# Kernel tuning notes

Measured on AMD Instinct MI355X. Metric: run time of the kernel, lower is better.

Reference implementation:

```python
import jax, jax.numpy as jnp
import numpy as np

B, T, D = 2, 4096, 1024      # batch, seq, hidden_dim
E, I = 16, 512               # n_routed_experts, expert_intermediate
K = 2                        # n_activated_experts
IS = 2048                    # shared_expert_intermediate
ALPHA = 1e-4                 # balance_loss_alpha
EPS = 1e-9


def setup_inputs() -> dict:
    key = jax.random.key(0)
    ks = jax.random.split(key, 8)
    s = lambda k, shape, fan: jax.random.normal(k, shape, jnp.float32) * (fan ** -0.5)
    return {
        "x": jax.random.normal(ks[0], (B, T, D), jnp.float32),
        "gate_w": s(ks[1], (D, E), D),            # router gate (no bias)
        "expert_bias": jnp.zeros((E,), jnp.float32),
        "sh_gate": s(ks[2], (D, IS), D),          # shared expert SwiGLU
        "sh_up": s(ks[3], (D, IS), D),
        "sh_down": s(ks[4], (IS, D), IS),
        "ex_gate": s(ks[5], (E, D, I), D),        # routed experts (stacked)
        "ex_up": s(ks[6], (E, D, I), D),
        "ex_down": s(ks[7], (E, I, D), I),
    }


def _swiglu(x, wg, wu, wd):
    return (jax.nn.silu(x @ wg) * (x @ wu)) @ wd


def reference(x, gate_w, expert_bias, sh_gate, sh_up, sh_down, ex_gate, ex_up, ex_down):
    Bq, Tq, Dq = x.shape
    # shared expert path (n_shared_experts = 1)
    shared = _swiglu(x, sh_gate, sh_up, sh_down)

    xf = x.reshape(Bq * Tq, Dq)                       # (N, D)
    N = xf.shape[0]

    # --- router: sigmoid gating, bias-adjusted top-k, normalized gates ---
    affinity = jax.nn.sigmoid(xf @ gate_w)            # (N, E)
    scores = affinity + expert_bias[None, :]
    _, idx = jax.lax.top_k(scores, K)                 # (N, K) int
    gv = jnp.take_along_axis(affinity, idx, axis=1)   # (N, K) gathered from affinity
    gv = gv / (gv.sum(-1, keepdims=True) + EPS)

    # --- balance loss (sequence-wise, Eq. 17-20) ---
    expert_mask = jax.nn.one_hot(idx, E, dtype=jnp.float32).sum(1)  # (N, E)
    f = expert_mask.sum(0) * E / (K * N)
    P = (affinity / (affinity.sum(-1, keepdims=True) + EPS)).mean(0)
    balance_loss = ALPHA * (f * P).sum()
    expert_counts = expert_mask.sum(0).astype(jnp.int32)            # (E,)

    # --- dispatch/compute/combine, expressed as dense combine-weight matrix ---
    # w[n, e] = sum of gate values for token n routed to expert e (same math
    # as the masked gather/scatter loop in the original)
    w = jnp.zeros((N, E), jnp.float32).at[jnp.arange(N)[:, None], idx].add(gv)
    h = jax.nn.silu(jnp.einsum('nd,edi->eni', xf, ex_gate)) \
        * jnp.einsum('nd,edi->eni', xf, ex_up)        # (E, N, I)
    routed = jnp.einsum('ne,eni,eid->nd', w, h, ex_down)  # (N, D)
    routed = routed.reshape(Bq, Tq, Dq)

    output = shared + routed  # note: original does NOT add residual despite docstring
    return output, balance_loss, expert_counts
```

## Files before the change

### kernel.cpp

```cpp
#include <hip/hip_runtime.h>
#include <stdint.h>

#define NTOK 8192
#define DDIM 1024
#define NEXP 16
#define KSEL 2
#define ISH 2048
#define IEX 512
#define ALPHAC 1e-4f
#define REPS 1e-9f

typedef __attribute__((ext_vector_type(8))) short short8;
typedef __attribute__((ext_vector_type(4))) float f32x4;

__device__ __forceinline__ unsigned short f2bf(float f){
  union { float f; uint32_t u; } v; v.f = f;
  uint32_t u = v.u;
  uint32_t r = (u + 0x7fffu + ((u >> 16) & 1u)) >> 16;
  return (unsigned short)r;
}
__device__ __forceinline__ float bf2f(unsigned short h){
  union { uint32_t u; float f; } v; v.u = ((uint32_t)h) << 16; return v.f;
}

__device__ __forceinline__ void gload16(const void* g, void* l){
  __builtin_amdgcn_global_load_lds(
      (const __attribute__((address_space(1))) void*)g,
      (__attribute__((address_space(3))) void*)l, 16, 0, 0);
}

__global__ __launch_bounds__(256) void convert_f32_bf16(const float* __restrict__ in,
                                                        unsigned short* __restrict__ out){
  int id = blockIdx.x * 256 + threadIdx.x;
  float4 v = ((const float4*)in)[id];
  ushort4 o;
  o.x = f2bf(v.x); o.y = f2bf(v.y); o.z = f2bf(v.z); o.w = f2bf(v.w);
  ((ushort4*)out)[id] = o;
}

__global__ __launch_bounds__(256) void transpose_bf16(const float* __restrict__ in,
                                                      unsigned short* __restrict__ outp,
                                                      int R, int C){
  __shared__ float tile[64][65];
  const size_t bofs = (size_t)blockIdx.z * R * C;
  const float* ip = in + bofs;
  unsigned short* op = outp + bofs;
  int c0 = blockIdx.x * 64, r0 = blockIdx.y * 64;
  int t = threadIdx.x;
  int tr = t >> 4, tc = (t & 15) * 4;
  #pragma unroll
  for (int i = 0; i < 4; ++i){
    float4 v = *(const float4*)&ip[(size_t)(r0 + tr + i*16) * C + c0 + tc];
    tile[tr + i*16][tc+0] = v.x;
    tile[tr + i*16][tc+1] = v.y;
    tile[tr + i*16][tc+2] = v.z;
    tile[tr + i*16][tc+3] = v.w;
  }
  __syncthreads();
  #pragma unroll
  for (int i = 0; i < 4; ++i){
    int oc = tr + i*16;
    ushort4 w;
    w.x = f2bf(tile[tc+0][oc]);
    w.y = f2bf(tile[tc+1][oc]);
    w.z = f2bf(tile[tc+2][oc]);
    w.w = f2bf(tile[tc+3][oc]);
    *(ushort4*)&op[(size_t)(c0 + oc) * R + r0 + tc] = w;
  }
}

__global__ __launch_bounds__(256) void logits_kernel(
    const float* __restrict__ x, const float* __restrict__ gw,
    float* __restrict__ logits)
{
  __shared__ float gws[16][1024];
  const int t = threadIdx.x;
  #pragma unroll
  for (int k = 0; k < 16; ++k){
    int idx = t + k * 256;
    float4 v = ((const float4*)gw)[idx];
    int d = idx >> 2, e0 = (idx & 3) * 4;
    gws[e0+0][d] = v.x;
    gws[e0+1][d] = v.y;
    gws[e0+2][d] = v.z;
    gws[e0+3][d] = v.w;
  }
  __syncthreads();
  const int lane = t & 63, w = t >> 6;
  const int nb = blockIdx.x * 16 + w * 4;
  for (int i = 0; i < 4; ++i){
    const int n = nb + i;
    const float4* xr = (const float4*)(x + (size_t)n * DDIM);
    float4 xv[4];
    #pragma unroll
    for (int k = 0; k < 4; ++k) xv[k] = xr[lane + k*64];
    float acc[16];
    #pragma unroll
    for (int e = 0; e < 16; ++e){
      float s = 0.f;
      #pragma unroll
      for (int k = 0; k < 4; ++k){
        float4 g = *(const float4*)&gws[e][(lane + k*64)*4];
        s = fmaf(xv[k].x, g.x, fmaf(xv[k].y, g.y, fmaf(xv[k].z, g.z, fmaf(xv[k].w, g.w, s))));
      }
      acc[e] = s;
    }
    #pragma unroll
    for (int m = 1; m < 64; m <<= 1)
      #pragma unroll
      for (int e = 0; e < 16; ++e)
        acc[e] += __shfl_xor(acc[e], m);
    if (lane == 0){
      float4* op = (float4*)(logits + (size_t)n * 16);
      op[0] = make_float4(acc[0],  acc[1],  acc[2],  acc[3]);
      op[1] = make_float4(acc[4],  acc[5],  acc[6],  acc[7]);
      op[2] = make_float4(acc[8],  acc[9],  acc[10], acc[11]);
      op[3] = make_float4(acc[12], acc[13], acc[14], acc[15]);
    }
  }
}

__global__ __launch_bounds__(256) void router_finish(
    const float* __restrict__ logits, const float* __restrict__ ebias,
    int* __restrict__ idxb, float* __restrict__ gvb,
    float* __restrict__ Ppart, int* __restrict__ Cpart)
{
  __shared__ float Ps[16];
  __shared__ int Cs[16];
  const int t = threadIdx.x;
  if (t < 16){ Ps[t] = 0.f; Cs[t] = 0; }
  __syncthreads();
  const int lane = t & 63;
  const int n = blockIdx.x * 256 + t;
  const float4* lp = (const float4*)(logits + (size_t)n * 16);
  float4 a0 = lp[0], a1 = lp[1], a2 = lp[2], a3 = lp[3];
  float aff[16];
  aff[0]=a0.x; aff[1]=a0.y; aff[2]=a0.z; aff[3]=a0.w;
  aff[4]=a1.x; aff[5]=a1.y; aff[6]=a1.z; aff[7]=a1.w;
  aff[8]=a2.x; aff[9]=a2.y; aff[10]=a2.z; aff[11]=a2.w;
  aff[12]=a3.x; aff[13]=a3.y; aff[14]=a3.z; aff[15]=a3.w;
  float rowsum = REPS;
  #pragma unroll
  for (int e = 0; e < 16; ++e){
    aff[e] = 1.f / (1.f + __expf(-aff[e]));
    rowsum += aff[e];
  }
  float bj[16];
  #pragma unroll
  for (int e = 0; e < 16; ++e) bj[e] = ebias[e];
  float bestS = aff[0] + bj[0], bestA = aff[0]; int i1 = 0;
  #pragma unroll
  for (int j = 1; j < 16; ++j){
    float sc = aff[j] + bj[j];
    bool gt2 = sc > bestS;
    bestS = gt2 ? sc : bestS; bestA = gt2 ? aff[j] : bestA; i1 = gt2 ? j : i1;
  }
  float secS = -1e30f, secA = 0.f; int i2 = 0;
  #pragma unroll
  for (int j = 0; j < 16; ++j){
    float sc = aff[j] + bj[j];
    bool ok = (j != i1) && (sc > secS);
    secS = ok ? sc : secS; secA = ok ? aff[j] : secA; i2 = ok ? j : i2;
  }
  float den = bestA + secA + REPS;
  idxb[n*2]   = i1; idxb[n*2+1] = i2;
  gvb[n*2]    = bestA / den; gvb[n*2+1] = secA / den;

  float inv = 1.f / rowsum;
  float pv[16]; int cv[16];
  #pragma unroll
  for (int e = 0; e < 16; ++e){
    pv[e] = aff[e] * inv;
    cv[e] = (e == i1) + (e == i2);
  }
  #pragma unroll
  for (int m = 1; m < 64; m <<= 1)
    #pragma unroll
    for (int e = 0; e < 16; ++e){
      pv[e] += __shfl_xor(pv[e], m);
      cv[e] += __shfl_xor(cv[e], m);
    }
  if (lane == 0){
    #pragma unroll
    for (int e = 0; e < 16; ++e){
      atomicAdd(&Ps[e], pv[e]);
      atomicAdd(&Cs[e], cv[e]);
    }
  }
  __syncthreads();
  if (t < 16){ Ppart[blockIdx.x*16 + t] = Ps[t]; Cpart[blockIdx.x*16 + t] = Cs[t]; }
}

__global__ __launch_bounds__(256) void finalize2(
    const float* __restrict__ Ppart, const int* __restrict__ Cpart,
    int* __restrict__ counts, int* __restrict__ offs, int* __restrict__ cursor,
    float* __restrict__ out_tail)
{
  __shared__ float P[16];
  __shared__ int C[16];
  int t = threadIdx.x;
  if (t < 16){ P[t] = 0.f; C[t] = 0; }
  __syncthreads();
  if (t < 32){
    int e = t & 15, c = t >> 4;
    float p = 0.f; int cc = 0;
    for (int b = c * 16; b < c * 16 + 16; ++b){ p += Ppart[b*16 + e]; cc += Cpart[b*16 + e]; }
    atomicAdd(&P[e], p); atomicAdd(&C[e], cc);
  }
  __syncthreads();
  if (t == 0){
    int a = 0; float loss = 0.f;
    for (int i = 0; i < 16; ++i){
      offs[i] = a; cursor[i] = a; counts[i] = C[i]; a += C[i];
      loss += ((float)C[i] * (float)NEXP / (float)(KSEL * NTOK)) * (P[i] / (float)NTOK);
      out_tail[1+i] = (float)C[i];
    }
    out_tail[0] = ALPHAC * loss;
  }
}

__global__ __launch_bounds__(256) void slot_assign(
    const int* __restrict__ idxb, const float* __restrict__ gvb,
    int* __restrict__ cursor, int* __restrict__ tokp, float* __restrict__ gatep,
    int* __restrict__ rslot)
{
  int i = blockIdx.x * 256 + threadIdx.x;
  int e = idxb[i];
  int s = atomicAdd(&cursor[e], 1);
  tokp[s] = i >> 1;
  gatep[s] = gvb[i];
  rslot[i] = s;
}

template<bool DUAL, bool GROUPED, bool GATHER, int OUT>
__global__ __launch_bounds__(256) void gemm128(
    const unsigned short* __restrict__ A,
    const unsigned short* __restrict__ B0,
    const unsigned short* __restrict__ B1,
    void* __restrict__ Cout,
    int M, int N, int K,
    const int* __restrict__ counts,
    const int* __restrict__ offsets,
    const int* __restrict__ perm,
    const float* __restrict__ rowscale)
{
  __shared__ __align__(16) unsigned short As [2][128*64];
  __shared__ __align__(16) unsigned short Bs0[2][128*64];
  __shared__ __align__(16) unsigned short Bs1[2][DUAL ? 128*64 : 8];

  const int bx = blockIdx.x, by = blockIdx.y;
  int mt = bx, off = 0, cnt = M;
  const unsigned short* b0p = B0;
  const unsigned short* b1p = B1;
  if (GROUPED){
    int acc = 0, e = -1;
    #pragma unroll
    for (int i = 0; i < NEXP; ++i){
      int c = counts[i]; int tt = (c + 127) >> 7;
      if (e < 0 && bx < acc + tt){ e = i; mt = bx - acc; off = offsets[i]; cnt = c; }
      acc += tt;
    }
    if (e < 0) return;
    b0p += (size_t)e * N * K;
    if (DUAL) b1p += (size_t)e * N * K;
  }
  const int m0 = mt * 128, n0 = by * 128;
  const int t = threadIdx.x;
  const int lane = t & 63;
  const int wid = t >> 6;
  const int wm = (wid >> 1) * 64;
  const int wn = (wid & 1) * 64;

  const unsigned short* asrc[4];
  const unsigned short* b0src[4];
  const unsigned short* b1src[4];
  int ldso[4];
  #pragma unroll
  for (int c = 0; c < 4; ++c){
    int s = (wid*4 + c)*64 + lane;
    int row = s >> 3, c16 = s & 7;
    int scol = c16 ^ (row & 7);
    ldso[c] = (wid*4 + c) * 512;
    int r = m0 + row;
    int rc = GROUPED ? (r < cnt ? r : cnt - 1) : r;
    int ar;
    if (GATHER) ar = perm[off + rc];
    else        ar = GROUPED ? off + rc : rc;
    asrc[c] = A + (size_t)ar * K + scol * 8;
    int br = n0 + row;
    b0src[c] = b0p + (size_t)br * K + scol * 8;
    if (DUAL) b1src[c] = b1p + (size_t)br * K + scol * 8;
  }

  f32x4 acc0[4][4];
  f32x4 acc1[4][4];
  #pragma unroll
  for (int i = 0; i < 4; ++i)
    #pragma unroll
    for (int j = 0; j < 4; ++j)
      #pragma unroll
      for (int r = 0; r < 4; ++r){ acc0[i][j][r] = 0.f; acc1[i][j][r] = 0.f; }

  const int l15 = lane & 15, g = lane >> 4;

  auto STAGE = [&](int buf, int k0){
    #pragma unroll
    for (int c = 0; c < 4; ++c){
      gload16(asrc[c]  + k0, (void*)&As [buf][ldso[c]]);
      gload16(b0src[c] + k0, (void*)&Bs0[buf][ldso[c]]);
      if (DUAL) gload16(b1src[c] + k0, (void*)&Bs1[buf][ldso[c]]);
    }
  };

  const int nt = K >> 6;
  STAGE(0, 0);
  __syncthreads();
  int cur = 0;
  for (int tk = 0; tk < nt; ++tk){
    if (tk + 1 < nt) STAGE(cur ^ 1, (tk + 1) << 6);
    #pragma unroll
    for (int ks = 0; ks < 2; ++ks){
      short8 af[4], bf0[4], bf1[4];
      #pragma unroll
      for (int i = 0; i < 4; ++i){
        int row = wm + i * 16 + l15;
        af[i] = *(const short8*)&As[cur][row * 64 + (((ks*4 + g) ^ (row & 7)) * 8)];
      }
      #pragma unroll
      for (int j = 0; j < 4; ++j){
        int row = wn + j * 16 + l15;
        bf0[j] = *(const short8*)&Bs0[cur][row * 64 + (((ks*4 + g) ^ (row & 7)) * 8)];
        if (DUAL) bf1[j] = *(const short8*)&Bs1[cur][row * 64 + (((ks*4 + g) ^ (row & 7)) * 8)];
      }
      #pragma unroll
      for (int i = 0; i < 4; ++i)
        #pragma unroll
        for (int j = 0; j < 4; ++j){
          acc0[i][j] = __builtin_amdgcn_mfma_f32_16x16x32_bf16(af[i], bf0[j], acc0[i][j], 0, 0, 0);
          if (DUAL)
            acc1[i][j] = __builtin_amdgcn_mfma_f32_16x16x32_bf16(af[i], bf1[j], acc1[i][j], 0, 0, 0);
        }
    }
    __syncthreads();
    cur ^= 1;
  }

  #pragma unroll
  for (int i = 0; i < 4; ++i)
    #pragma unroll
    for (int j = 0; j < 4; ++j)
      #pragma unroll
      for (int r = 0; r < 4; ++r){
        int lr = wm + i * 16 + g * 4 + r;
        int grow = m0 + lr;
        if (GROUPED && grow >= cnt) continue;
        int gcol = n0 + wn + j * 16 + l15;
        float val;
        if (DUAL){
          float gt = acc0[i][j][r];
          float up = acc1[i][j][r];
          val = gt / (1.f + __expf(-gt)) * up;
        } else {
          val = acc0[i][j][r];
        }
        if (OUT == 2) val *= rowscale[off + grow];
        size_t orow = GROUPED ? (size_t)(off + grow) : (size_t)grow;
        if (OUT == 1) ((float*)Cout)[orow * N + gcol] = val;
        else          ((unsigned short*)Cout)[orow * N + gcol] = f2bf(val);
      }
}

__global__ __launch_bounds__(256) void combine_kernel(float* __restrict__ out,
                                                      const unsigned short* __restrict__ ybuf,
                                                      const int* __restrict__ rs){
  int id = blockIdx.x * 256 + threadIdx.x;
  int n = id >> 8;
  int q = id & 255;
  int s0 = rs[n*2], s1 = rs[n*2+1];
  float4 o = ((float4*)out)[id];
  ushort4 a = ((const ushort4*)(ybuf + (size_t)s0 * DDIM))[q];
  ushort4 b = ((const ushort4*)(ybuf + (size_t)s1 * DDIM))[q];
  o.x += bf2f(a.x) + bf2f(b.x);
  o.y += bf2f(a.y) + bf2f(b.y);
  o.z += bf2f(a.z) + bf2f(b.z);
  o.w += bf2f(a.w) + bf2f(b.w);
  ((float4*)out)[id] = o;
}

extern "C" void kernel_launch(void* const* d_in, const int* in_sizes, int n_in,
                              void* d_out, int out_size, void* d_ws, size_t ws_size,
                              hipStream_t stream)
{
  const float* x       = (const float*)d_in[0];
  const float* gate_w  = (const float*)d_in[1];
  const float* ebias   = (const float*)d_in[2];
  const float* sh_gate = (const float*)d_in[3];
  const float* sh_up   = (const float*)d_in[4];
  const float* sh_down = (const float*)d_in[5];
  const float* ex_gate = (const float*)d_in[6];
  const float* ex_up   = (const float*)d_in[7];
  const float* ex_down = (const float*)d_in[8];
  float* out = (float*)d_out;
  (void)in_sizes; (void)n_in; (void)out_size; (void)ws_size;

  size_t o = 0;
  auto alloc = [&](size_t bytes) -> void* {
    o = (o + 255) & ~(size_t)255;
    void* p = (char*)d_ws + o;
    o += bytes;
    return p;
  };
  unsigned short* xb   = (unsigned short*)alloc((size_t)NTOK*DDIM*2);
  unsigned short* shgT = (unsigned short*)alloc((size_t)ISH*DDIM*2);
  unsigned short* shuT = (unsigned short*)alloc((size_t)ISH*DDIM*2);
  unsigned short* shdT = (unsigned short*)alloc((size_t)DDIM*ISH*2);
  unsigned short* exgT = (unsigned short*)alloc((size_t)NEXP*IEX*DDIM*2);
  unsigned short* exuT = (unsigned short*)alloc((size_t)NEXP*IEX*DDIM*2);
  unsigned short* exdT = (unsigned short*)alloc((size_t)NEXP*DDIM*IEX*2);
  unsigned short* hbuf = (unsigned short*)alloc((size_t)NTOK*KSEL*IEX*2);
  unsigned short* big  = (unsigned short*)alloc((size_t)NTOK*ISH*2);
  float* logits = (float*)alloc((size_t)NTOK*NEXP*4);
  int*   idxb  = (int*)alloc(NTOK*KSEL*4);
  float* gvb   = (float*)alloc(NTOK*KSEL*4);
  float* Ppart = (float*)alloc(32*16*4);
  int*   Cpart = (int*)alloc(32*16*4);
  int*   counts= (int*)alloc(64);
  int*   offs  = (int*)alloc(64);
  int*   cursor= (int*)alloc(64);
  int*   tokp  = (int*)alloc(NTOK*KSEL*4);
  float* gatep = (float*)alloc(NTOK*KSEL*4);
  int*   rslot = (int*)alloc(NTOK*KSEL*4);

  convert_f32_bf16<<<NTOK*DDIM/1024, 256, 0, stream>>>(x, xb);
  transpose_bf16<<<dim3(ISH/64,  DDIM/64, 1),    256, 0, stream>>>(sh_gate, shgT, DDIM, ISH);
  transpose_bf16<<<dim3(ISH/64,  DDIM/64, 1),    256, 0, stream>>>(sh_up,   shuT, DDIM, ISH);
  transpose_bf16<<<dim3(DDIM/64, ISH/64,  1),    256, 0, stream>>>(sh_down, shdT, ISH, DDIM);
  transpose_bf16<<<dim3(IEX/64,  DDIM/64, NEXP), 256, 0, stream>>>(ex_gate, exgT, DDIM, IEX);
  transpose_bf16<<<dim3(IEX/64,  DDIM/64, NEXP), 256, 0, stream>>>(ex_up,   exuT, DDIM, IEX);
  transpose_bf16<<<dim3(DDIM/64, IEX/64,  NEXP), 256, 0, stream>>>(ex_down, exdT, IEX, DDIM);

  logits_kernel<<<512, 256, 0, stream>>>(x, gate_w, logits);
  router_finish<<<32, 256, 0, stream>>>(logits, ebias, idxb, gvb, Ppart, Cpart);
  finalize2<<<1, 256, 0, stream>>>(Ppart, Cpart, counts, offs, cursor,
                                   out + (size_t)NTOK*DDIM);
  slot_assign<<<NTOK*KSEL/256, 256, 0, stream>>>(idxb, gvb, cursor, tokp, gatep, rslot);

  gemm128<true,false,false,0><<<dim3(NTOK/128, ISH/128), 256, 0, stream>>>(
      xb, shgT, shuT, big, NTOK, ISH, DDIM, nullptr, nullptr, nullptr, nullptr);
  gemm128<false,false,false,1><<<dim3(NTOK/128, DDIM/128), 256, 0, stream>>>(
      big, shdT, nullptr, out, NTOK, DDIM, ISH, nullptr, nullptr, nullptr, nullptr);

  gemm128<true,true,true,0><<<dim3(144, IEX/128), 256, 0, stream>>>(
      xb, exgT, exuT, hbuf, 0, IEX, DDIM, counts, offs, tokp, nullptr);
  gemm128<false,true,false,2><<<dim3(144, DDIM/128), 256, 0, stream>>>(
      hbuf, exdT, nullptr, big, 0, DDIM, IEX, counts, offs, nullptr, gatep);

  combine_kernel<<<NTOK*DDIM/1024, 256, 0, stream>>>(out, big, rslot);
}
```

Before: 451.9 us.

## Split dual gate/up GEMM into two single GEMMs to raise occupancy

The fused gate+up SwiGLU GEMM, which held two accumulator sets and two B tiles in LDS, is replaced by two single-B GEMM launches. The first writes silu(gate) as bf16 and the second multiplies its up result by that stored value in the epilogue. Launch bounds now request two blocks per CU, aiming for more waves resident via lower register and LDS use. In exchange A is loaded twice, the intermediate makes an extra global round-trip, and silu(gate) is rounded to bf16 before the multiply.

```diff
diff --git a/kernel.cpp b/kernel.cpp
--- a/kernel.cpp
+++ b/kernel.cpp
@@ -232,11 +232,11 @@
   rslot[i] = s;
 }
 
-template<bool DUAL, bool GROUPED, bool GATHER, int OUT>
-__global__ __launch_bounds__(256) void gemm128(
+template<bool GROUPED, bool GATHER, int MODE>
+__global__ __launch_bounds__(256, 2) void gemm128(
     const unsigned short* __restrict__ A,
-    const unsigned short* __restrict__ B0,
-    const unsigned short* __restrict__ B1,
+    const unsigned short* __restrict__ B,
+    const unsigned short* __restrict__ comp,
     void* __restrict__ Cout,
     int M, int N, int K,
     const int* __restrict__ counts,
@@ -244,14 +244,12 @@
     const int* __restrict__ perm,
     const float* __restrict__ rowscale)
 {
-  __shared__ __align__(16) unsigned short As [2][128*64];
-  __shared__ __align__(16) unsigned short Bs0[2][128*64];
-  __shared__ __align__(16) unsigned short Bs1[2][DUAL ? 128*64 : 8];
+  __shared__ __align__(16) unsigned short As[2][128*64];
+  __shared__ __align__(16) unsigned short Bs[2][128*64];
 
   const int bx = blockIdx.x, by = blockIdx.y;
   int mt = bx, off = 0, cnt = M;
-  const unsigned short* b0p = B0;
-  const unsigned short* b1p = B1;
+  const unsigned short* bp = B;
   if (GROUPED){
     int acc = 0, e = -1;
     #pragma unroll
@@ -261,8 +259,7 @@
       acc += tt;
     }
     if (e < 0) return;
-    b0p += (size_t)e * N * K;
-    if (DUAL) b1p += (size_t)e * N * K;
+    bp += (size_t)e * N * K;
   }
   const int m0 = mt * 128, n0 = by * 128;
   const int t = threadIdx.x;
@@ -270,46 +267,39 @@
   const int wid = t >> 6;
   const int wm = (wid >> 1) * 64;
   const int wn = (wid & 1) * 64;
+  const int l15 = lane & 15, g = lane >> 4;
 
   const unsigned short* asrc[4];
-  const unsigned short* b0src[4];
-  const unsigned short* b1src[4];
+  const unsigned short* bsrc[4];
   int ldso[4];
   #pragma unroll
   for (int c = 0; c < 4; ++c){
     int s = (wid*4 + c)*64 + lane;
     int row = s >> 3, c16 = s & 7;
-    int scol = c16 ^ (row & 7);
+    int scol = (c16 ^ (row & 7)) * 8;
     ldso[c] = (wid*4 + c) * 512;
     int r = m0 + row;
-    int rc = GROUPED ? (r < cnt ? r : cnt - 1) : r;
+    int rc = GROUPED ? (r < cnt ? r : (cnt > 0 ? cnt - 1 : 0)) : r;
     int ar;
     if (GATHER) ar = perm[off + rc];
     else        ar = GROUPED ? off + rc : rc;
-    asrc[c] = A + (size_t)ar * K + scol * 8;
-    int br = n0 + row;
-    b0src[c] = b0p + (size_t)br * K + scol * 8;
-    if (DUAL) b1src[c] = b1p + (size_t)br * K + scol * 8;
-  }
-
-  f32x4 acc0[4][4];
-  f32x4 acc1[4][4];
+    asrc[c] = A + (size_t)ar * K + scol;
+    bsrc[c] = bp + (size_t)(n0 + row) * K + scol;
+  }
+
+  f32x4 acc[4][4];
   #pragma unroll
   for (int i = 0; i < 4; ++i)
     #pragma unroll
     for (int j = 0; j < 4; ++j)
       #pragma unroll
-      for (int r = 0; r < 4; ++r){ acc0[i][j][r] = 0.f; acc1[i][j][r] = 0.f; }
-
-  const int l15 = lane & 15, g = lane >> 4;
+      for (int r = 0; r < 4; ++r) acc[i][j][r] = 0.f;
 
   auto STAGE = [&](int buf, int k0){
     #pragma unroll
-    for (int c = 0; c < 4; ++c){
-      gload16(asrc[c]  + k0, (void*)&As [buf][ldso[c]]);
-      gload16(b0src[c] + k0, (void*)&Bs0[buf][ldso[c]]);
-      if (DUAL) gload16(b1src[c] + k0, (void*)&Bs1[buf][ldso[c]]);
-    }
+    for (int c = 0; c < 4; ++c) gload16(asrc[c] + k0, (void*)&As[buf][ldso[c]]);
+    #pragma unroll
+    for (int c = 0; c < 4; ++c) gload16(bsrc[c] + k0, (void*)&Bs[buf][ldso[c]]);
   };
 
   const int nt = K >> 6;
@@ -320,7 +310,7 @@
     if (tk + 1 < nt) STAGE(cur ^ 1, (tk + 1) << 6);
     #pragma unroll
     for (int ks = 0; ks < 2; ++ks){
-      short8 af[4], bf0[4], bf1[4];
+      short8 af[4], bf[4];
       #pragma unroll
       for (int i = 0; i < 4; ++i){
         int row = wm + i * 16 + l15;
@@ -329,17 +319,13 @@
       #pragma unroll
       for (int j = 0; j < 4; ++j){
         int row = wn + j * 16 + l15;
-        bf0[j] = *(const short8*)&Bs0[cur][row * 64 + (((ks*4 + g) ^ (row & 7)) * 8)];
-        if (DUAL) bf1[j] = *(const short8*)&Bs1[cur][row * 64 + (((ks*4 + g) ^ (row & 7)) * 8)];
+        bf[j] = *(const short8*)&Bs[cur][row * 64 + (((ks*4 + g) ^ (row & 7)) * 8)];
       }
       #pragma unroll
       for (int i = 0; i < 4; ++i)
         #pragma unroll
-        for (int j = 0; j < 4; ++j){
-          acc0[i][j] = __builtin_amdgcn_mfma_f32_16x16x32_bf16(af[i], bf0[j], acc0[i][j], 0, 0, 0);
-          if (DUAL)
-            acc1[i][j] = __builtin_amdgcn_mfma_f32_16x16x32_bf16(af[i], bf1[j], acc1[i][j], 0, 0, 0);
-        }
+        for (int j = 0; j < 4; ++j)
+          acc[i][j] = __builtin_amdgcn_mfma_f32_16x16x32_bf16(af[i], bf[j], acc[i][j], 0, 0, 0);
     }
     __syncthreads();
     cur ^= 1;
@@ -355,18 +341,16 @@
         int grow = m0 + lr;
         if (GROUPED && grow >= cnt) continue;
         int gcol = n0 + wn + j * 16 + l15;
-        float val;
-        if (DUAL){
-          float gt = acc0[i][j][r];
-          float up = acc1[i][j][r];
-          val = gt / (1.f + __expf(-gt)) * up;
+        size_t orow = GROUPED ? (size_t)(off + grow) : (size_t)grow;
+        float val = acc[i][j][r];
+        if (MODE == 1){
+          ((float*)Cout)[orow * N + gcol] = val;
         } else {
-          val = acc0[i][j][r];
+          if (MODE == 2) val *= rowscale[off + grow];
+          if (MODE == 4) val = val / (1.f + __expf(-val));
+          if (MODE == 5) val *= bf2f(comp[orow * N + gcol]);
+          ((unsigned short*)Cout)[orow * N + gcol] = f2bf(val);
         }
-        if (OUT == 2) val *= rowscale[off + grow];
-        size_t orow = GROUPED ? (size_t)(off + grow) : (size_t)grow;
-        if (OUT == 1) ((float*)Cout)[orow * N + gcol] = val;
-        else          ((unsigned short*)Cout)[orow * N + gcol] = f2bf(val);
       }
 }
 
@@ -445,14 +429,18 @@
                                    out + (size_t)NTOK*DDIM);
   slot_assign<<<NTOK*KSEL/256, 256, 0, stream>>>(idxb, gvb, cursor, tokp, gatep, rslot);
 
-  gemm128<true,false,false,0><<<dim3(NTOK/128, ISH/128), 256, 0, stream>>>(
-      xb, shgT, shuT, big, NTOK, ISH, DDIM, nullptr, nullptr, nullptr, nullptr);
-  gemm128<false,false,false,1><<<dim3(NTOK/128, DDIM/128), 256, 0, stream>>>(
+  gemm128<false,false,4><<<dim3(NTOK/128, ISH/128), 256, 0, stream>>>(
+      xb, shgT, nullptr, big, NTOK, ISH, DDIM, nullptr, nullptr, nullptr, nullptr);
+  gemm128<false,false,5><<<dim3(NTOK/128, ISH/128), 256, 0, stream>>>(
+      xb, shuT, big, big, NTOK, ISH, DDIM, nullptr, nullptr, nullptr, nullptr);
+  gemm128<false,false,1><<<dim3(NTOK/128, DDIM/128), 256, 0, stream>>>(
       big, shdT, nullptr, out, NTOK, DDIM, ISH, nullptr, nullptr, nullptr, nullptr);
 
-  gemm128<true,true,true,0><<<dim3(144, IEX/128), 256, 0, stream>>>(
-      xb, exgT, exuT, hbuf, 0, IEX, DDIM, counts, offs, tokp, nullptr);
-  gemm128<false,true,false,2><<<dim3(144, DDIM/128), 256, 0, stream>>>(
+  gemm128<true,true,4><<<dim3(144, IEX/128), 256, 0, stream>>>(
+      xb, exgT, nullptr, hbuf, 0, IEX, DDIM, counts, offs, tokp, nullptr);
+  gemm128<true,true,5><<<dim3(144, IEX/128), 256, 0, stream>>>(
+      xb, exuT, hbuf, hbuf, 0, IEX, DDIM, counts, offs, tokp, nullptr);
+  gemm128<true,false,2><<<dim3(144, DDIM/128), 256, 0, stream>>>(
       hbuf, exdT, nullptr, big, 0, DDIM, IEX, counts, offs, nullptr, gatep);
 
   combine_kernel<<<NTOK*DDIM/1024, 256, 0, stream>>>(out, big, rslot);
```

New measurement: 458.2 us. Within noise of the previous version (+1.4%).
